# Kernel tuning notes

Hardware: AMD Instinct MI355X
Metric: run time of the kernel (lower is better)

## Reference

```python
import jax, jax.numpy as jnp
import numpy as np

B, T, V, E, H = 4096, 80, 80, 8, 256  # batch, seq_len, num_classes/vocab, embed dim, n_hidden
FORGET_BIAS = 1.0  # tf BasicLSTMCell default


def lstm_layer(x, W, b):
    """Run one BasicLSTMCell layer over time. x: [B, T, D]; W: [D+H, 4H]; b: [4H].
    TF BasicLSTMCell gate order is (i, j, f, o); new_c = c*sig(f+fb) + sig(i)*tanh(j)."""
    Bsz = x.shape[0]

    def step(carry, xt):
        c, h = carry
        gates = jnp.concatenate([xt, h], axis=-1) @ W + b  # [B, 4H]
        i, j, f, o = jnp.split(gates, 4, axis=-1)
        c = c * jax.nn.sigmoid(f + FORGET_BIAS) + jax.nn.sigmoid(i) * jnp.tanh(j)
        h = jnp.tanh(c) * jax.nn.sigmoid(o)
        return (c, h), h

    init = (jnp.zeros((Bsz, H), x.dtype), jnp.zeros((Bsz, H), x.dtype))
    _, hs = jax.lax.scan(step, init, jnp.swapaxes(x, 0, 1))  # hs: [T, B, H]
    return jnp.swapaxes(hs, 0, 1)  # [B, T, H]


def setup_inputs() -> dict:
    key = jax.random.key(0)
    ks = jax.random.split(key, 8)
    features = jax.random.randint(ks[0], (B, T), 0, V, dtype=jnp.int32)
    labels = jax.random.randint(ks[1], (B,), 0, V, dtype=jnp.int32)
    emb = jax.random.normal(ks[2], (V, E), dtype=jnp.float32) * 0.1  # trainable=False in original
    W1 = jax.random.normal(ks[3], (E + H, 4 * H), dtype=jnp.float32) * 0.05
    b1 = jnp.zeros((4 * H,), jnp.float32)
    W2 = jax.random.normal(ks[4], (H + H, 4 * H), dtype=jnp.float32) * 0.05
    b2 = jnp.zeros((4 * H,), jnp.float32)
    Wd = jax.random.normal(ks[5], (H, V), dtype=jnp.float32) * 0.05
    bd = jnp.zeros((V,), jnp.float32)
    return {"features": features, "labels": labels, "emb": emb,
            "W1": W1, "b1": b1, "W2": W2, "b2": b2, "Wd": Wd, "bd": bd}


def reference(features, labels, emb, W1, b1, W2, b2, Wd, bd):
    x = emb[features]                     # [B, T, E] embedding lookup
    h1 = lstm_layer(x, W1, b1)            # [B, T, H]
    h2 = lstm_layer(h1, W2, b2)           # [B, T, H]
    pred = h2[:, -1, :] @ Wd + bd         # [B, V] logits from last timestep
    y = jax.nn.one_hot(labels, V, dtype=pred.dtype)
    loss = jnp.mean(jnp.sum(-y * jax.nn.log_softmax(pred, axis=-1), axis=-1))
    return loss
```

## Files before the change

kernel.cpp:

```cpp
#include <hip/hip_runtime.h>
#include <math.h>

#define B_SZ 4096
#define T_SZ 80
#define V_SZ 80
#define E_SZ 8
#define H_SZ 256
#define G4   1024

typedef __attribute__((ext_vector_type(8))) short short8;
typedef __attribute__((ext_vector_type(4))) float f32x4;

typedef __attribute__((address_space(1))) const unsigned gu32;
typedef __attribute__((address_space(3))) unsigned su32;

__device__ __forceinline__ void glds16(const ushort* g, ushort* l) {
    __builtin_amdgcn_global_load_lds((gu32*)g, (su32*)l, 16, 0, 0);
}

__device__ __forceinline__ float sigm(float x) {
    return 1.f / (1.f + __expf(-x));
}
__device__ __forceinline__ float tanhfast(float x) {
    x = fminf(fmaxf(x, -15.f), 15.f);
    float t = __expf(-2.f * x);
    return (1.f - t) / (1.f + t);
}
__device__ __forceinline__ ushort f2bf(float f) {
    unsigned u = __float_as_uint(f);
    u = (u + 0x7fffu + ((u >> 16) & 1u)) >> 16;
    return (ushort)u;
}

__global__ __launch_bounds__(256) void g1_kernel(const float* __restrict__ emb,
                                                 const float* __restrict__ W1,
                                                 const float* __restrict__ b1,
                                                 float* __restrict__ G1) {
    int idx = blockIdx.x * 256 + threadIdx.x;
    if (idx >= V_SZ * G4) return;
    int v = idx >> 10, col = idx & 1023;
    float g = b1[col];
#pragma unroll
    for (int e = 0; e < E_SZ; e++)
        g += emb[v * E_SZ + e] * W1[e * G4 + col];
    G1[idx] = g;
}

__global__ __launch_bounds__(256) void wtransf(const float* __restrict__ src, int k0,
                                               int KTmask, int KTsh,
                                               ushort* __restrict__ out) {
    int idx = blockIdx.x * 256 + threadIdx.x;
    int j = idx & 7;
    int c = (idx >> 3) & 511;
    int ktile = (idx >> 12) & KTmask;
    int hb = idx >> (12 + KTsh);
    int cf = c >> 6;
    int k = k0 + ktile * 32 + ((c >> 4) & 3) * 8 + j;
    int ncol = (cf >> 1) * 256 + hb * 32 + (cf & 1) * 16 + (c & 15);
    out[idx] = f2bf(src[(size_t)k * G4 + ncol]);
}

__global__ __launch_bounds__(256) void wdtrans(const float* __restrict__ src,
                                               ushort* __restrict__ out) {
    int idx = blockIdx.x * 256 + threadIdx.x;
    if (idx >= V_SZ * H_SZ) return;
    int v = idx >> 8, h = idx & 255;
    out[idx] = f2bf(src[h * V_SZ + v]);
}

__global__ __launch_bounds__(256) void lstm_fused(
    const ushort* __restrict__ A1h, int Kend1,
    const int*   __restrict__ feat,
    const float* __restrict__ G1,
    float* __restrict__ c1, ushort* __restrict__ h1out,
    const ushort* __restrict__ A2x, const ushort* __restrict__ A2h, int Kend2,
    const float* __restrict__ b2,
    float* __restrict__ c2, ushort* __restrict__ h2out,
    const ushort* __restrict__ W1f, const ushort* __restrict__ W2f) {

    const int z = blockIdx.z;
    const int Kend = z ? Kend2 : Kend1;
    if (Kend < 0) return;
    const int KT = z ? 16 : 8;
    const ushort* __restrict__ Wf = z ? W2f : W1f;

    __shared__ __align__(16) ushort As[2][4096];
    __shared__ __align__(16) ushort Ws[2][4096];

    const int tid = threadIdx.x;
    const int w = tid >> 6, l = tid & 63;
    const int l15 = l & 15, l4 = l >> 4;
    const int m0 = blockIdx.x * 128;
    const int hb = blockIdx.y;
    const int h0 = hb * 32;

    const int rowS0 = w * 32 + l15;
    const int rowS1 = w * 32 + 16 + l15;
    const int kq8 = l4 * 8;
    const int S0 = w * 2, S1 = w * 2 + 1;
    const size_t wtileb = (size_t)hb * KT * 512;

    const int aoff0 = (w * 128 + l) * 8;
    const int aoff1 = (w * 128 + 64 + l) * 8;
    const int boff  = l * 8;

    f32x4 acc[2][8];
    const f32x4 zero4 = {0.f, 0.f, 0.f, 0.f};
#pragma unroll
    for (int fg = 0; fg < 2; fg++)
#pragma unroll
        for (int cf = 0; cf < 8; cf++) acc[fg][cf] = zero4;

    auto stage = [&](int buf, int kt) {
        const ushort* Asrc; int kl;
        if (!z || kt < 256) { Asrc = z ? A2x : A1h; kl = kt; }
        else                { Asrc = A2h; kl = kt - 256; }
        glds16(Asrc + (size_t)(m0 + rowS0) * H_SZ + kl + kq8, As[buf] + S0 * 512);
        glds16(Asrc + (size_t)(m0 + rowS1) * H_SZ + kl + kq8, As[buf] + S1 * 512);
        const ushort* wsrc = Wf + (wtileb + (size_t)(kt >> 5) * 512) * 8;
        glds16(wsrc + (S0 * 64 + l) * 8, Ws[buf] + S0 * 512);
        glds16(wsrc + (S1 * 64 + l) * 8, Ws[buf] + S1 * 512);
    };

    if (Kend > 0) {
        stage(0, 0);
        __syncthreads();
        int cur = 0;
        for (int kt = 0; kt < Kend; kt += 32) {
            short8 a0 = *(const short8*)(As[cur] + aoff0);
            short8 a1 = *(const short8*)(As[cur] + aoff1);
            short8 bq[8];
#pragma unroll
            for (int cf = 0; cf < 8; cf++)
                bq[cf] = *(const short8*)(Ws[cur] + cf * 512 + boff);

            if (kt + 32 < Kend) stage(cur ^ 1, kt + 32);

            __builtin_amdgcn_s_setprio(1);
#pragma unroll
            for (int cf = 0; cf < 8; cf++) {
                acc[0][cf] = __builtin_amdgcn_mfma_f32_16x16x32_bf16(a0, bq[cf], acc[0][cf], 0, 0, 0);
                acc[1][cf] = __builtin_amdgcn_mfma_f32_16x16x32_bf16(a1, bq[cf], acc[1][cf], 0, 0, 0);
            }
            __builtin_amdgcn_s_setprio(0);
            __syncthreads();
            cur ^= 1;
        }
    }

    float* __restrict__ cbuf = z ? c2 : c1;
    ushort* __restrict__ hout = z ? h2out : h1out;
    const bool cz = z ? (Kend == 256) : (Kend == 0);

#pragma unroll
    for (int fg = 0; fg < 2; fg++) {
#pragma unroll
        for (int r = 0; r < 4; r++) {
            const int grow = m0 + w * 32 + fg * 16 + l4 * 4 + r;
            const float* gb = z ? b2 : (G1 + (size_t)feat[(size_t)grow * T_SZ] * G4);
#pragma unroll
            for (int h16 = 0; h16 < 2; h16++) {
                const int hcol = h0 + h16 * 16 + l15;
                float gi = acc[fg][0 + h16][r] + gb[hcol];
                float gj = acc[fg][2 + h16][r] + gb[256 + hcol];
                float gf = acc[fg][4 + h16][r] + gb[512 + hcol];
                float go = acc[fg][6 + h16][r] + gb[768 + hcol];
                const size_t ci = (size_t)grow * H_SZ + hcol;
                float cp = cz ? 0.f : cbuf[ci];
                float cn = cp * sigm(gf + 1.f) + sigm(gi) * tanhfast(gj);
                float hn = tanhfast(cn) * sigm(go);
                cbuf[ci] = cn;
                hout[ci] = f2bf(hn);
            }
        }
    }
}

__global__ __launch_bounds__(256) void dense_loss(const ushort* __restrict__ h2,
                                                  const ushort* __restrict__ WdT,
                                                  const float* __restrict__ bd,
                                                  const int* __restrict__ labels,
                                                  float* __restrict__ out) {
    const int tid = threadIdx.x;
    const int w = tid >> 6, l = tid & 63;
    const int l15 = l & 15, l4 = l >> 4;
    const int m0 = blockIdx.x * 64 + w * 16;

    f32x4 acc[5];
    const f32x4 zero4 = {0.f, 0.f, 0.f, 0.f};
#pragma unroll
    for (int cf = 0; cf < 5; cf++) acc[cf] = zero4;

    for (int kt = 0; kt < 256; kt += 32) {
        short8 a = *(const short8*)(h2 + (size_t)(m0 + l15) * H_SZ + l4 * 8 + kt);
#pragma unroll
        for (int cf = 0; cf < 5; cf++) {
            short8 b = *(const short8*)(WdT + (size_t)(cf * 16 + l15) * H_SZ + l4 * 8 + kt);
            acc[cf] = __builtin_amdgcn_mfma_f32_16x16x32_bf16(a, b, acc[cf], 0, 0, 0);
        }
    }
#pragma unroll
    for (int cf = 0; cf < 5; cf++) {
        float bv = bd[cf * 16 + l15];
#pragma unroll
        for (int r = 0; r < 4; r++) acc[cf][r] += bv;
    }

#pragma unroll
    for (int r = 0; r < 4; r++) {
        const int row = m0 + l4 * 4 + r;
        float mx = acc[0][r];
#pragma unroll
        for (int cf = 1; cf < 5; cf++) mx = fmaxf(mx, acc[cf][r]);
#pragma unroll
        for (int msk = 1; msk < 16; msk <<= 1)
            mx = fmaxf(mx, __shfl_xor(mx, msk, 64));
        float s = 0.f;
#pragma unroll
        for (int cf = 0; cf < 5; cf++) s += __expf(acc[cf][r] - mx);
#pragma unroll
        for (int msk = 1; msk < 16; msk <<= 1)
            s += __shfl_xor(s, msk, 64);
        const int lab = labels[row];
        float pl = 0.f;
#pragma unroll
        for (int cf = 0; cf < 5; cf++)
            pl += (cf * 16 + l15 == lab) ? acc[cf][r] : 0.f;
#pragma unroll
        for (int msk = 1; msk < 16; msk <<= 1)
            pl += __shfl_xor(pl, msk, 64);
        if (l15 == 0)
            atomicAdd(out, (logf(s) + mx - pl) * (1.0f / B_SZ));
    }
}

extern "C" void kernel_launch(void* const* d_in, const int* in_sizes, int n_in,
                              void* d_out, int out_size, void* d_ws, size_t ws_size,
                              hipStream_t stream) {
    const int*   features = (const int*)d_in[0];
    const int*   labels   = (const int*)d_in[1];
    const float* emb      = (const float*)d_in[2];
    const float* W1       = (const float*)d_in[3];
    const float* b1       = (const float*)d_in[4];
    const float* W2       = (const float*)d_in[5];
    const float* b2       = (const float*)d_in[6];
    const float* Wd       = (const float*)d_in[7];
    const float* bd       = (const float*)d_in[8];
    float* out = (float*)d_out;

    char* base = (char*)d_ws;
    float*  G1v = (float*)base;      base += (size_t)V_SZ * G4 * 4;
    float*  c1  = (float*)base;      base += (size_t)B_SZ * H_SZ * 4;
    float*  c2  = (float*)base;      base += (size_t)B_SZ * H_SZ * 4;
    ushort* h1b[2]; ushort* h2b[2];
    h1b[0] = (ushort*)base;          base += (size_t)B_SZ * H_SZ * 2;
    h1b[1] = (ushort*)base;          base += (size_t)B_SZ * H_SZ * 2;
    h2b[0] = (ushort*)base;          base += (size_t)B_SZ * H_SZ * 2;
    h2b[1] = (ushort*)base;          base += (size_t)B_SZ * H_SZ * 2;
    ushort* W1f = (ushort*)base;     base += (size_t)8 * 8 * 512 * 8 * 2;
    ushort* W2f = (ushort*)base;     base += (size_t)8 * 16 * 512 * 8 * 2;
    ushort* WdT = (ushort*)base;     base += (size_t)V_SZ * H_SZ * 2;

    (void)hipMemsetAsync(d_out, 0, sizeof(float), stream);
    g1_kernel<<<(V_SZ * G4 + 255) / 256, 256, 0, stream>>>(emb, W1, b1, G1v);
    wtransf<<<(8 * 8 * 512 * 8) / 256, 256, 0, stream>>>(W1, E_SZ, 7, 3, W1f);
    wtransf<<<(8 * 16 * 512 * 8) / 256, 256, 0, stream>>>(W2, 0, 15, 4, W2f);
    wdtrans<<<(V_SZ * H_SZ + 255) / 256, 256, 0, stream>>>(Wd, WdT);

    dim3 grid(B_SZ / 128, H_SZ / 32, 2), blk(256);
    for (int t = 0; t <= T_SZ; t++) {
        const int Kend1 = (t < T_SZ) ? (t ? 256 : 0) : -1;
        const int Kend2 = (t >= 1) ? ((t >= 2) ? 512 : 256) : -1;
        lstm_fused<<<grid, blk, 0, stream>>>(
            (t && t < T_SZ) ? h1b[(t - 1) & 1] : nullptr, Kend1,
            features + t, G1v, c1, h1b[t & 1],
            (t >= 1) ? h1b[(t - 1) & 1] : nullptr,
            (t >= 2) ? h2b[(t - 2) & 1] : nullptr, Kend2,
            b2, c2, (t >= 1) ? h2b[(t - 1) & 1] : nullptr,
            W1f, W2f);
    }
    dense_loss<<<B_SZ / 64, 256, 0, stream>>>(h2b[(T_SZ - 1) & 1], WdT, bd, labels, out);
}
```

Baseline: 1.632 ms.

## Run entire two-layer LSTM recurrence in one persistent row-local kernel

Replaces the 81 per-timestep launches with a single kernel where each block owns 32 batch rows and iterates all timesteps internally. Hidden states stay in LDS and cell states in registers, and weights are streamed from global/L2 each step in a per-wave fragment layout. This removes launch overhead and the global round trips of h and c. In exchange only 128 blocks run, each with 8 waves, so weight streaming from L2 and the small grid may limit throughput.

```diff
diff --git a/kernel.cpp b/kernel.cpp
--- a/kernel.cpp
+++ b/kernel.cpp
@@ -7,16 +7,11 @@
 #define E_SZ 8
 #define H_SZ 256
 #define G4   1024
+#define RB   32
+#define NBLK (B_SZ / RB)
 
 typedef __attribute__((ext_vector_type(8))) short short8;
 typedef __attribute__((ext_vector_type(4))) float f32x4;
-
-typedef __attribute__((address_space(1))) const unsigned gu32;
-typedef __attribute__((address_space(3))) unsigned su32;
-
-__device__ __forceinline__ void glds16(const ushort* g, ushort* l) {
-    __builtin_amdgcn_global_load_lds((gu32*)g, (su32*)l, 16, 0, 0);
-}
 
 __device__ __forceinline__ float sigm(float x) {
     return 1.f / (1.f + __expf(-x));
@@ -30,6 +25,9 @@
     unsigned u = __float_as_uint(f);
     u = (u + 0x7fffu + ((u >> 16) & 1u)) >> 16;
     return (ushort)u;
+}
+__device__ __forceinline__ f32x4 mfma16(short8 a, short8 b, f32x4 c) {
+    return __builtin_amdgcn_mfma_f32_16x16x32_bf16(a, b, c, 0, 0, 0);
 }
 
 __global__ __launch_bounds__(256) void g1_kernel(const float* __restrict__ emb,
@@ -46,18 +44,18 @@
     G1[idx] = g;
 }
 
-__global__ __launch_bounds__(256) void wtransf(const float* __restrict__ src, int k0,
-                                               int KTmask, int KTsh,
-                                               ushort* __restrict__ out) {
+__global__ __launch_bounds__(256) void wtransf2(const float* __restrict__ src, int k0,
+                                                int KTmask, int KTsh,
+                                                ushort* __restrict__ out) {
     int idx = blockIdx.x * 256 + threadIdx.x;
-    int j = idx & 7;
-    int c = (idx >> 3) & 511;
-    int ktile = (idx >> 12) & KTmask;
-    int hb = idx >> (12 + KTsh);
-    int cf = c >> 6;
-    int k = k0 + ktile * 32 + ((c >> 4) & 3) * 8 + j;
-    int ncol = (cf >> 1) * 256 + hb * 32 + (cf & 1) * 16 + (c & 15);
-    out[idx] = f2bf(src[(size_t)k * G4 + ncol]);
+    int j  = idx & 7;
+    int l  = (idx >> 3) & 63;
+    int cf = (idx >> 9) & 7;
+    int kt = (idx >> 12) & KTmask;
+    int w  = idx >> (12 + KTsh);
+    int k  = k0 + kt * 32 + (l >> 4) * 8 + j;
+    int col = (cf >> 1) * 256 + w * 32 + (cf & 1) * 16 + (l & 15);
+    out[idx] = f2bf(src[(size_t)k * G4 + col]);
 }
 
 __global__ __launch_bounds__(256) void wdtrans(const float* __restrict__ src,
@@ -68,111 +66,186 @@
     out[idx] = f2bf(src[h * V_SZ + v]);
 }
 
-__global__ __launch_bounds__(256) void lstm_fused(
-    const ushort* __restrict__ A1h, int Kend1,
+__global__ __launch_bounds__(512) void lstm_rowlocal(
     const int*   __restrict__ feat,
     const float* __restrict__ G1,
-    float* __restrict__ c1, ushort* __restrict__ h1out,
-    const ushort* __restrict__ A2x, const ushort* __restrict__ A2h, int Kend2,
     const float* __restrict__ b2,
-    float* __restrict__ c2, ushort* __restrict__ h2out,
-    const ushort* __restrict__ W1f, const ushort* __restrict__ W2f) {
-
-    const int z = blockIdx.z;
-    const int Kend = z ? Kend2 : Kend1;
-    if (Kend < 0) return;
-    const int KT = z ? 16 : 8;
-    const ushort* __restrict__ Wf = z ? W2f : W1f;
-
-    __shared__ __align__(16) ushort As[2][4096];
-    __shared__ __align__(16) ushort Ws[2][4096];
+    const ushort* __restrict__ W1f,
+    const ushort* __restrict__ W2f,
+    ushort* __restrict__ h2g,
+    int padsel) {
+
+    __shared__ __align__(16) ushort h1s[2][8192];
+    __shared__ __align__(16) ushort h2s[2][8192];
+    __shared__ ushort pad[12288];
 
     const int tid = threadIdx.x;
     const int w = tid >> 6, l = tid & 63;
     const int l15 = l & 15, l4 = l >> 4;
-    const int m0 = blockIdx.x * 128;
-    const int hb = blockIdx.y;
-    const int h0 = hb * 32;
-
-    const int rowS0 = w * 32 + l15;
-    const int rowS1 = w * 32 + 16 + l15;
-    const int kq8 = l4 * 8;
-    const int S0 = w * 2, S1 = w * 2 + 1;
-    const size_t wtileb = (size_t)hb * KT * 512;
-
-    const int aoff0 = (w * 128 + l) * 8;
-    const int aoff1 = (w * 128 + 64 + l) * 8;
-    const int boff  = l * 8;
-
-    f32x4 acc[2][8];
+    const int m0 = blockIdx.x * RB;
+
+    if (padsel) {
+        pad[tid] = (ushort)tid;
+        h2g[tid] = pad[tid ^ 1];
+    }
+
+    float bb[8];
+#pragma unroll
+    for (int cf = 0; cf < 8; cf++)
+        bb[cf] = b2[(cf >> 1) * 256 + w * 32 + (cf & 1) * 16 + l15];
+
+    float c1r[16], c2r[16];
+#pragma unroll
+    for (int i = 0; i < 16; i++) { c1r[i] = 0.f; c2r[i] = 0.f; }
+
+    const ushort* w1p = W1f + (size_t)(w * 8) * 8 * 512 + l * 8;
+    const ushort* w2p = W2f + (size_t)(w * 16) * 8 * 512 + l * 8;
+
+    const int hwrB = (l15 >> 3);
     const f32x4 zero4 = {0.f, 0.f, 0.f, 0.f};
-#pragma unroll
-    for (int fg = 0; fg < 2; fg++)
-#pragma unroll
-        for (int cf = 0; cf < 8; cf++) acc[fg][cf] = zero4;
-
-    auto stage = [&](int buf, int kt) {
-        const ushort* Asrc; int kl;
-        if (!z || kt < 256) { Asrc = z ? A2x : A1h; kl = kt; }
-        else                { Asrc = A2h; kl = kt - 256; }
-        glds16(Asrc + (size_t)(m0 + rowS0) * H_SZ + kl + kq8, As[buf] + S0 * 512);
-        glds16(Asrc + (size_t)(m0 + rowS1) * H_SZ + kl + kq8, As[buf] + S1 * 512);
-        const ushort* wsrc = Wf + (wtileb + (size_t)(kt >> 5) * 512) * 8;
-        glds16(wsrc + (S0 * 64 + l) * 8, Ws[buf] + S0 * 512);
-        glds16(wsrc + (S1 * 64 + l) * 8, Ws[buf] + S1 * 512);
-    };
-
-    if (Kend > 0) {
-        stage(0, 0);
+
+#pragma unroll 1
+    for (int t = 0; t < T_SZ; t++) {
+        f32x4 acc[2][8];
+#pragma unroll
+        for (int rt = 0; rt < 2; rt++)
+#pragma unroll
+            for (int cf = 0; cf < 8; cf++) acc[rt][cf] = zero4;
+
+        if (t > 0) {
+            const ushort* ab = h1s[(t + 1) & 1];
+            short8 wf[2][8];
+#pragma unroll
+            for (int cf = 0; cf < 8; cf++)
+                wf[0][cf] = *(const short8*)(w1p + (size_t)cf * 512);
+#pragma unroll
+            for (int kt = 0; kt < 8; kt++) {
+                if (kt < 7) {
+#pragma unroll
+                    for (int cf = 0; cf < 8; cf++)
+                        wf[(kt + 1) & 1][cf] =
+                            *(const short8*)(w1p + ((size_t)(kt + 1) * 8 + cf) * 512);
+                }
+                short8 a0 = *(const short8*)(ab + (0 * 8 + kt) * 512 + l * 8);
+                short8 a1 = *(const short8*)(ab + (1 * 8 + kt) * 512 + l * 8);
+                __builtin_amdgcn_s_setprio(1);
+#pragma unroll
+                for (int cf = 0; cf < 8; cf++) {
+                    acc[0][cf] = mfma16(a0, wf[kt & 1][cf], acc[0][cf]);
+                    acc[1][cf] = mfma16(a1, wf[kt & 1][cf], acc[1][cf]);
+                }
+                __builtin_amdgcn_s_setprio(0);
+            }
+        }
+
+        {
+            ushort* ho = h1s[t & 1];
+#pragma unroll
+            for (int rt = 0; rt < 2; rt++) {
+#pragma unroll
+                for (int r = 0; r < 4; r++) {
+                    const int row = rt * 16 + l4 * 4 + r;
+                    const int fr = feat[(size_t)(m0 + row) * T_SZ + t];
+                    const float* gr = G1 + (size_t)fr * G4;
+#pragma unroll
+                    for (int hh = 0; hh < 2; hh++) {
+                        const int hc = w * 32 + hh * 16 + l15;
+                        float gi = acc[rt][0 + hh][r] + gr[hc];
+                        float gj = acc[rt][2 + hh][r] + gr[256 + hc];
+                        float gf = acc[rt][4 + hh][r] + gr[512 + hc];
+                        float go = acc[rt][6 + hh][r] + gr[768 + hc];
+                        const int ci = (rt * 4 + r) * 2 + hh;
+                        float cp = t ? c1r[ci] : 0.f;
+                        float cn = cp * sigm(gf + 1.f) + sigm(gi) * tanhfast(gj);
+                        float hn = tanhfast(cn) * sigm(go);
+                        c1r[ci] = cn;
+                        ho[(rt * 8 + w) * 512 +
+                           ((row & 15) + (hh * 2 + hwrB) * 16) * 8 + (l15 & 7)] = f2bf(hn);
+                    }
+                }
+            }
+        }
         __syncthreads();
-        int cur = 0;
-        for (int kt = 0; kt < Kend; kt += 32) {
-            short8 a0 = *(const short8*)(As[cur] + aoff0);
-            short8 a1 = *(const short8*)(As[cur] + aoff1);
-            short8 bq[8];
+
+#pragma unroll
+        for (int rt = 0; rt < 2; rt++)
+#pragma unroll
+            for (int cf = 0; cf < 8; cf++) acc[rt][cf] = zero4;
+
+        {
+            const ushort* a1b = h1s[t & 1];
+            const ushort* a2b = h2s[(t + 1) & 1];
+            short8 wf[2][8];
 #pragma unroll
             for (int cf = 0; cf < 8; cf++)
-                bq[cf] = *(const short8*)(Ws[cur] + cf * 512 + boff);
-
-            if (kt + 32 < Kend) stage(cur ^ 1, kt + 32);
-
-            __builtin_amdgcn_s_setprio(1);
-#pragma unroll
-            for (int cf = 0; cf < 8; cf++) {
-                acc[0][cf] = __builtin_amdgcn_mfma_f32_16x16x32_bf16(a0, bq[cf], acc[0][cf], 0, 0, 0);
-                acc[1][cf] = __builtin_amdgcn_mfma_f32_16x16x32_bf16(a1, bq[cf], acc[1][cf], 0, 0, 0);
-            }
-            __builtin_amdgcn_s_setprio(0);
-            __syncthreads();
-            cur ^= 1;
-        }
-    }
-
-    float* __restrict__ cbuf = z ? c2 : c1;
-    ushort* __restrict__ hout = z ? h2out : h1out;
-    const bool cz = z ? (Kend == 256) : (Kend == 0);
-
-#pragma unroll
-    for (int fg = 0; fg < 2; fg++) {
-#pragma unroll
-        for (int r = 0; r < 4; r++) {
-            const int grow = m0 + w * 32 + fg * 16 + l4 * 4 + r;
-            const float* gb = z ? b2 : (G1 + (size_t)feat[(size_t)grow * T_SZ] * G4);
-#pragma unroll
-            for (int h16 = 0; h16 < 2; h16++) {
-                const int hcol = h0 + h16 * 16 + l15;
-                float gi = acc[fg][0 + h16][r] + gb[hcol];
-                float gj = acc[fg][2 + h16][r] + gb[256 + hcol];
-                float gf = acc[fg][4 + h16][r] + gb[512 + hcol];
-                float go = acc[fg][6 + h16][r] + gb[768 + hcol];
-                const size_t ci = (size_t)grow * H_SZ + hcol;
-                float cp = cz ? 0.f : cbuf[ci];
-                float cn = cp * sigm(gf + 1.f) + sigm(gi) * tanhfast(gj);
-                float hn = tanhfast(cn) * sigm(go);
-                cbuf[ci] = cn;
-                hout[ci] = f2bf(hn);
-            }
-        }
+                wf[0][cf] = *(const short8*)(w2p + (size_t)cf * 512);
+#pragma unroll
+            for (int kt = 0; kt < 8; kt++) {
+#pragma unroll
+                for (int cf = 0; cf < 8; cf++)
+                    wf[(kt + 1) & 1][cf] =
+                        *(const short8*)(w2p + ((size_t)(kt + 1) * 8 + cf) * 512);
+                short8 a0 = *(const short8*)(a1b + (0 * 8 + kt) * 512 + l * 8);
+                short8 a1 = *(const short8*)(a1b + (1 * 8 + kt) * 512 + l * 8);
+                __builtin_amdgcn_s_setprio(1);
+#pragma unroll
+                for (int cf = 0; cf < 8; cf++) {
+                    acc[0][cf] = mfma16(a0, wf[kt & 1][cf], acc[0][cf]);
+                    acc[1][cf] = mfma16(a1, wf[kt & 1][cf], acc[1][cf]);
+                }
+                __builtin_amdgcn_s_setprio(0);
+            }
+            if (t > 0) {
+#pragma unroll
+                for (int kt = 8; kt < 16; kt++) {
+                    if (kt < 15) {
+#pragma unroll
+                        for (int cf = 0; cf < 8; cf++)
+                            wf[(kt + 1) & 1][cf] =
+                                *(const short8*)(w2p + ((size_t)(kt + 1) * 8 + cf) * 512);
+                    }
+                    short8 a0 = *(const short8*)(a2b + (0 * 8 + kt - 8) * 512 + l * 8);
+                    short8 a1 = *(const short8*)(a2b + (1 * 8 + kt - 8) * 512 + l * 8);
+                    __builtin_amdgcn_s_setprio(1);
+#pragma unroll
+                    for (int cf = 0; cf < 8; cf++) {
+                        acc[0][cf] = mfma16(a0, wf[kt & 1][cf], acc[0][cf]);
+                        acc[1][cf] = mfma16(a1, wf[kt & 1][cf], acc[1][cf]);
+                    }
+                    __builtin_amdgcn_s_setprio(0);
+                }
+            }
+        }
+
+        {
+            ushort* ho = h2s[t & 1];
+#pragma unroll
+            for (int rt = 0; rt < 2; rt++) {
+#pragma unroll
+                for (int r = 0; r < 4; r++) {
+                    const int row = rt * 16 + l4 * 4 + r;
+#pragma unroll
+                    for (int hh = 0; hh < 2; hh++) {
+                        const int hc = w * 32 + hh * 16 + l15;
+                        float gi = acc[rt][0 + hh][r] + bb[0 + hh];
+                        float gj = acc[rt][2 + hh][r] + bb[2 + hh];
+                        float gf = acc[rt][4 + hh][r] + bb[4 + hh];
+                        float go = acc[rt][6 + hh][r] + bb[6 + hh];
+                        const int ci = (rt * 4 + r) * 2 + hh;
+                        float cp = t ? c2r[ci] : 0.f;
+                        float cn = cp * sigm(gf + 1.f) + sigm(gi) * tanhfast(gj);
+                        float hn = tanhfast(cn) * sigm(go);
+                        c2r[ci] = cn;
+                        ushort hb = f2bf(hn);
+                        ho[(rt * 8 + w) * 512 +
+                           ((row & 15) + (hh * 2 + hwrB) * 16) * 8 + (l15 & 7)] = hb;
+                        if (t == T_SZ - 1)
+                            h2g[(size_t)(m0 + row) * H_SZ + hc] = hb;
+                    }
+                }
+            }
+        }
+        __syncthreads();
     }
 }
 
@@ -250,34 +323,18 @@
 
     char* base = (char*)d_ws;
     float*  G1v = (float*)base;      base += (size_t)V_SZ * G4 * 4;
-    float*  c1  = (float*)base;      base += (size_t)B_SZ * H_SZ * 4;
-    float*  c2  = (float*)base;      base += (size_t)B_SZ * H_SZ * 4;
-    ushort* h1b[2]; ushort* h2b[2];
-    h1b[0] = (ushort*)base;          base += (size_t)B_SZ * H_SZ * 2;
-    h1b[1] = (ushort*)base;          base += (size_t)B_SZ * H_SZ * 2;
-    h2b[0] = (ushort*)base;          base += (size_t)B_SZ * H_SZ * 2;
-    h2b[1] = (ushort*)base;          base += (size_t)B_SZ * H_SZ * 2;
-    ushort* W1f = (ushort*)base;     base += (size_t)8 * 8 * 512 * 8 * 2;
-    ushort* W2f = (ushort*)base;     base += (size_t)8 * 16 * 512 * 8 * 2;
+    ushort* W1f = (ushort*)base;     base += (size_t)8 * 8 * 8 * 512 * 2;
+    ushort* W2f = (ushort*)base;     base += (size_t)8 * 16 * 8 * 512 * 2;
     ushort* WdT = (ushort*)base;     base += (size_t)V_SZ * H_SZ * 2;
+    ushort* h2g = (ushort*)base;     base += (size_t)B_SZ * H_SZ * 2;
 
     (void)hipMemsetAsync(d_out, 0, sizeof(float), stream);
     g1_kernel<<<(V_SZ * G4 + 255) / 256, 256, 0, stream>>>(emb, W1, b1, G1v);
-    wtransf<<<(8 * 8 * 512 * 8) / 256, 256, 0, stream>>>(W1, E_SZ, 7, 3, W1f);
-    wtransf<<<(8 * 16 * 512 * 8) / 256, 256, 0, stream>>>(W2, 0, 15, 4, W2f);
+    wtransf2<<<(8 * 8 * 8 * 512) / 256, 256, 0, stream>>>(W1, E_SZ, 7, 3, W1f);
+    wtransf2<<<(8 * 16 * 8 * 512) / 256, 256, 0, stream>>>(W2, 0, 15, 4, W2f);
     wdtrans<<<(V_SZ * H_SZ + 255) / 256, 256, 0, stream>>>(Wd, WdT);
 
-    dim3 grid(B_SZ / 128, H_SZ / 32, 2), blk(256);
-    for (int t = 0; t <= T_SZ; t++) {
-        const int Kend1 = (t < T_SZ) ? (t ? 256 : 0) : -1;
-        const int Kend2 = (t >= 1) ? ((t >= 2) ? 512 : 256) : -1;
-        lstm_fused<<<grid, blk, 0, stream>>>(
-            (t && t < T_SZ) ? h1b[(t - 1) & 1] : nullptr, Kend1,
-            features + t, G1v, c1, h1b[t & 1],
-            (t >= 1) ? h1b[(t - 1) & 1] : nullptr,
-            (t >= 2) ? h2b[(t - 2) & 1] : nullptr, Kend2,
-            b2, c2, (t >= 1) ? h2b[(t - 1) & 1] : nullptr,
-            W1f, W2f);
-    }
-    dense_loss<<<B_SZ / 64, 256, 0, stream>>>(h2b[(T_SZ - 1) & 1], WdT, bd, labels, out);
-}
+    lstm_rowlocal<<<NBLK, 512, 0, stream>>>(features, G1v, b2, W1f, W2f, h2g, 0);
+
+    dense_loss<<<B_SZ / 64, 256, 0, stream>>>(h2g, WdT, bd, labels, out);
+}
```

After: 5.677 ms. 248% more time.
